# Kernel optimization log

Hardware: AMD Instinct MI355X
Metric: run time of the kernel (lower is better)

## Reference

```python
import jax, jax.numpy as jnp
import numpy as np
import math

N = 12288
D = 64
SCALE0 = math.log(10.0)


def lorentz_linear(x, W, b, scale):
    # x: [N, D] -> nn.Linear then Lorentz re-normalization onto the hyperboloid
    h = x @ W.T + b
    time = jax.nn.sigmoid(h[:, :1]) * jnp.exp(scale) + 1.1  # [N, 1]
    xn = h[:, 1:]  # spatial components [N, D-1]
    sq = jnp.clip(jnp.sum(xn * xn, axis=-1, keepdims=True), 1e-8, None)
    s = (time * time - 1.0) / sq
    return jnp.concatenate([time, xn * jnp.sqrt(s)], axis=-1)


def setup_inputs() -> dict:
    key = jax.random.key(0)
    ks = jax.random.split(key, 8)
    stdv = 1.0 / math.sqrt(D)
    x = jax.random.normal(ks[0], (N, D), dtype=jnp.float32)
    # sparse-ish binary adjacency stored dense (module calls adj.to_dense())
    adj = (jax.random.uniform(ks[1], (N, N)) < 0.002).astype(jnp.float32)
    W = jax.random.uniform(ks[2], (D, D), minval=-stdv, maxval=stdv, dtype=jnp.float32)
    Wq = jax.random.uniform(ks[3], (D, D), minval=-stdv, maxval=stdv, dtype=jnp.float32)
    Wk = jax.random.uniform(ks[4], (D, D), minval=-stdv, maxval=stdv, dtype=jnp.float32)
    z = jnp.zeros((D,), dtype=jnp.float32)
    sc = jnp.asarray(SCALE0, dtype=jnp.float32)
    return {
        'x': x, 'adj': adj,
        'W': W, 'b': z, 'scale': sc,
        'Wq': Wq, 'bq': z, 'scale_q': sc,
        'Wk': Wk, 'bk': z, 'scale_k': sc,
        'att_bias': jnp.asarray(20.0, dtype=jnp.float32),
        'att_scale': jnp.asarray(math.sqrt(D), dtype=jnp.float32),
    }


def reference(x, adj, W, b, scale, Wq, bq, scale_q, Wk, bk, scale_k, att_bias, att_scale):
    # LorentzLinear
    h = lorentz_linear(x, W, b, scale)  # [N, D]
    # LorentzAgg with attention
    q = lorentz_linear(h, Wq, bq, scale_q)
    k = lorentz_linear(h, Wk, bk, scale_k)
    # cinner: Lorentzian inner product matrix (negate time component of q)
    qm = jnp.concatenate([-q[:, :1], q[:, 1:]], axis=-1)
    att = 2.0 + 2.0 * (qm @ k.T)                 # [N, N]
    att = jax.nn.sigmoid(att / att_scale + att_bias)
    att = adj * att                               # mask by adjacency
    support = att @ h                             # [N, D]
    # Lorentz self-inner: inner(v,v) = -v0^2 + sum(v_rest^2); denorm = sqrt(|-inner|)
    inner = -support[:, :1] ** 2 + jnp.sum(support[:, 1:] ** 2, axis=-1, keepdims=True)
    denorm = jnp.sqrt(jnp.clip(jnp.abs(-inner), 1e-8, None))
    return support / denorm
```

## Files before the change

kernel.cpp:

```cpp
#include <hip/hip_runtime.h>
#include <math.h>

#define N   12288
#define D   64
#define CAP 96

typedef unsigned int uint4n __attribute__((ext_vector_type(4)));

__device__ __forceinline__ float wave_sum(float v) {
    #pragma unroll
    for (int m = 32; m >= 1; m >>= 1) v += __shfl_xor(v, m, 64);
    return v;
}
__device__ __forceinline__ float sigmoidf(float a) { return 1.0f / (1.0f + __expf(-a)); }

__global__ __launch_bounds__(256) void phase1_kernel(
        const float* __restrict__ x,
        const uint4n* __restrict__ adj4,
        const float* __restrict__ W,  const float* __restrict__ b,  const float* __restrict__ scale,
        const float* __restrict__ Wq, const float* __restrict__ bq, const float* __restrict__ scale_q,
        const float* __restrict__ Wk, const float* __restrict__ bk, const float* __restrict__ scale_k,
        float* __restrict__ h, float* __restrict__ qm, float* __restrict__ kmat,
        int* __restrict__ cnt, int* __restrict__ cols) {
    __shared__ float Wl [D * (D + 1)];
    __shared__ float Wql[D * (D + 1)];
    __shared__ float Wkl[D * (D + 1)];
    __shared__ unsigned short scols[4][CAP];
    __shared__ int scnt[4];

    const int tid  = threadIdx.x;
    const int lane = tid & 63;
    const int w    = tid >> 6;
    const int row  = blockIdx.x * 4 + w;

    for (int idx = tid; idx < D * D; idx += 256) {
        int d = idx >> 6, kk = idx & 63;
        Wl [d * (D + 1) + kk] = W [idx];
        Wql[d * (D + 1) + kk] = Wq[idx];
        Wkl[d * (D + 1) + kk] = Wk[idx];
    }
    if (lane == 0) scnt[w] = 0;
    __syncthreads();

    float hvv;
    {
        float xv  = x[row * D + lane];
        float acc = b[lane];
        const float* wr = &Wl[lane * (D + 1)];
        #pragma unroll
        for (int kk = 0; kk < D; ++kk)
            acc = fmaf(__shfl(xv, kk, 64), wr[kk], acc);
        float h0   = __shfl(acc, 0, 64);
        float time = __expf(scale[0]) * sigmoidf(h0) + 1.1f;
        float sq   = fmaxf(wave_sum((lane == 0) ? 0.0f : acc * acc), 1e-8f);
        float r    = sqrtf((time * time - 1.0f) / sq);
        hvv = (lane == 0) ? time : acc * r;
        h[row * D + lane] = hvv;
    }

    {
        float accq = bq[lane], acck = bk[lane];
        const float* wq = &Wql[lane * (D + 1)];
        const float* wk = &Wkl[lane * (D + 1)];
        #pragma unroll
        for (int kk = 0; kk < D; ++kk) {
            float xk = __shfl(hvv, kk, 64);
            accq = fmaf(xk, wq[kk], accq);
            acck = fmaf(xk, wk[kk], acck);
        }
        {
            float h0   = __shfl(accq, 0, 64);
            float time = __expf(scale_q[0]) * sigmoidf(h0) + 1.1f;
            float sq   = fmaxf(wave_sum((lane == 0) ? 0.0f : accq * accq), 1e-8f);
            float r    = sqrtf((time * time - 1.0f) / sq);
            qm[row * D + lane] = (lane == 0) ? -time : accq * r;
        }
        {
            float h0   = __shfl(acck, 0, 64);
            float time = __expf(scale_k[0]) * sigmoidf(h0) + 1.1f;
            float sq   = fmaxf(wave_sum((lane == 0) ? 0.0f : acck * acck), 1e-8f);
            float r    = sqrtf((time * time - 1.0f) / sq);
            kmat[row * D + lane] = (lane == 0) ? time : acck * r;
        }
    }

    {
        const uint4n* rp = adj4 + (size_t)row * (N / 4);
        #pragma unroll 4
        for (int it = 0; it < (N / 4) / 64; ++it) {
            int t = it * 64 + lane;
            uint4n v = __builtin_nontemporal_load(&rp[t]);
            if ((v.x | v.y | v.z | v.w) != 0u) {
                unsigned e[4] = {v.x, v.y, v.z, v.w};
                #pragma unroll
                for (int c = 0; c < 4; ++c) {
                    if (e[c] != 0u) {
                        int pos = atomicAdd(&scnt[w], 1);
                        if (pos < CAP) scols[w][pos] = (unsigned short)(t * 4 + c);
                    }
                }
            }
        }
        int m = scnt[w]; if (m > CAP) m = CAP;
        if (lane == 0) cnt[row] = m;
        for (int n = lane; n < m; n += 64)
            cols[row * CAP + n] = scols[w][n];
    }
}

__global__ __launch_bounds__(256) void gather_kernel(
        const float* __restrict__ qm,
        const float* __restrict__ kmat,
        const float* __restrict__ h,
        const int* __restrict__ cnt,
        const int* __restrict__ cols,
        const float* __restrict__ att_bias_p,
        const float* __restrict__ att_scale_p,
        float* __restrict__ out) {
    int lane = threadIdx.x & 63;
    int row  = blockIdx.x * 4 + (threadIdx.x >> 6);

    float qv = qm[row * D + lane];
    int m = cnt[row];
    float bias      = att_bias_p[0];
    float inv_scale = 1.0f / att_scale_p[0];

    float acc = 0.0f;
    for (int n = 0; n < m; ++n) {
        int j = cols[row * CAP + n];
        float dot = wave_sum(qv * kmat[j * D + lane]);
        float att = sigmoidf(fmaf(2.0f + 2.0f * dot, inv_scale, bias));
        acc = fmaf(att, h[j * D + lane], acc);
    }

    float contrib = (lane == 0) ? -acc * acc : acc * acc;
    float inner   = wave_sum(contrib);
    float denorm  = sqrtf(fmaxf(fabsf(inner), 1e-8f));
    out[row * D + lane] = acc / denorm;
}

extern "C" void kernel_launch(void* const* d_in, const int* in_sizes, int n_in,
                              void* d_out, int out_size, void* d_ws, size_t ws_size,
                              hipStream_t stream) {
    const float*  x         = (const float*)d_in[0];
    const uint4n* adj       = (const uint4n*)d_in[1];
    const float*  W         = (const float*)d_in[2];
    const float*  b         = (const float*)d_in[3];
    const float*  scale     = (const float*)d_in[4];
    const float*  Wq        = (const float*)d_in[5];
    const float*  bq        = (const float*)d_in[6];
    const float*  scale_q   = (const float*)d_in[7];
    const float*  Wk        = (const float*)d_in[8];
    const float*  bk        = (const float*)d_in[9];
    const float*  scale_k   = (const float*)d_in[10];
    const float*  att_bias  = (const float*)d_in[11];
    const float*  att_scale = (const float*)d_in[12];
    float* out = (float*)d_out;

    float* h    = (float*)d_ws;
    float* qm   = h    + (size_t)N * D;
    float* kmat = qm   + (size_t)N * D;
    int*   cnt  = (int*)(kmat + (size_t)N * D);
    int*   cols = cnt + N;

    phase1_kernel<<<N / 4, 256, 0, stream>>>(x, adj, W, b, scale,
                                             Wq, bq, scale_q, Wk, bk, scale_k,
                                             h, qm, kmat, cnt, cols);
    gather_kernel<<<N / 4, 256, 0, stream>>>(qm, kmat, h, cnt, cols,
                                             att_bias, att_scale, out);
}
```

Measured before the change: 851.5 us.

## Fuse adjacency scan into gather kernel with one block per row

Moves the dense adjacency row scan out of the linear kernel and into the gather kernel. Each 256-thread block now scans one row and keeps the neighbor list in shared memory. The four waves then split the neighbor loop and reduce their partial sums through shared memory. This drops the global cols/cnt round trip and spreads the scan of the 600MB adjacency over more waves per row. The cost is an extra block barrier, a cross-wave reduction, and three idle waves during the final normalization.

```diff
diff --git a/kernel.cpp b/kernel.cpp
--- a/kernel.cpp
+++ b/kernel.cpp
@@ -14,19 +14,15 @@
 }
 __device__ __forceinline__ float sigmoidf(float a) { return 1.0f / (1.0f + __expf(-a)); }
 
-__global__ __launch_bounds__(256) void phase1_kernel(
+__global__ __launch_bounds__(256) void linear_kernel(
         const float* __restrict__ x,
-        const uint4n* __restrict__ adj4,
         const float* __restrict__ W,  const float* __restrict__ b,  const float* __restrict__ scale,
         const float* __restrict__ Wq, const float* __restrict__ bq, const float* __restrict__ scale_q,
         const float* __restrict__ Wk, const float* __restrict__ bk, const float* __restrict__ scale_k,
-        float* __restrict__ h, float* __restrict__ qm, float* __restrict__ kmat,
-        int* __restrict__ cnt, int* __restrict__ cols) {
+        float* __restrict__ h, float* __restrict__ qm, float* __restrict__ kmat) {
     __shared__ float Wl [D * (D + 1)];
     __shared__ float Wql[D * (D + 1)];
     __shared__ float Wkl[D * (D + 1)];
-    __shared__ unsigned short scols[4][CAP];
-    __shared__ int scnt[4];
 
     const int tid  = threadIdx.x;
     const int lane = tid & 63;
@@ -39,7 +35,6 @@
         Wql[d * (D + 1) + kk] = Wq[idx];
         Wkl[d * (D + 1) + kk] = Wk[idx];
     }
-    if (lane == 0) scnt[w] = 0;
     __syncthreads();
 
     float hvv;
@@ -83,60 +78,68 @@
             kmat[row * D + lane] = (lane == 0) ? time : acck * r;
         }
     }
+}
 
-    {
-        const uint4n* rp = adj4 + (size_t)row * (N / 4);
-        #pragma unroll 4
-        for (int it = 0; it < (N / 4) / 64; ++it) {
-            int t = it * 64 + lane;
-            uint4n v = __builtin_nontemporal_load(&rp[t]);
-            if ((v.x | v.y | v.z | v.w) != 0u) {
-                unsigned e[4] = {v.x, v.y, v.z, v.w};
-                #pragma unroll
-                for (int c = 0; c < 4; ++c) {
-                    if (e[c] != 0u) {
-                        int pos = atomicAdd(&scnt[w], 1);
-                        if (pos < CAP) scols[w][pos] = (unsigned short)(t * 4 + c);
-                    }
+__global__ __launch_bounds__(256) void adj_gather_kernel(
+        const uint4n* __restrict__ adj4,
+        const float* __restrict__ qm,
+        const float* __restrict__ kmat,
+        const float* __restrict__ h,
+        const float* __restrict__ att_bias_p,
+        const float* __restrict__ att_scale_p,
+        float* __restrict__ out) {
+    __shared__ int scols[CAP];
+    __shared__ int scnt;
+    __shared__ float sacc[4][D];
+
+    int tid  = threadIdx.x;
+    int row  = blockIdx.x;
+    if (tid == 0) scnt = 0;
+    __syncthreads();
+
+    const uint4n* rowp = adj4 + (size_t)row * (N / 4);
+    #pragma unroll
+    for (int it = 0; it < (N / 4) / 256; ++it) {
+        int t = it * 256 + tid;
+        uint4n v = __builtin_nontemporal_load(&rowp[t]);
+        if ((v.x | v.y | v.z | v.w) != 0u) {
+            unsigned e[4] = {v.x, v.y, v.z, v.w};
+            #pragma unroll
+            for (int c = 0; c < 4; ++c) {
+                if (e[c] != 0u) {
+                    int pos = atomicAdd(&scnt, 1);
+                    if (pos < CAP) scols[pos] = t * 4 + c;
                 }
             }
         }
-        int m = scnt[w]; if (m > CAP) m = CAP;
-        if (lane == 0) cnt[row] = m;
-        for (int n = lane; n < m; n += 64)
-            cols[row * CAP + n] = scols[w][n];
     }
-}
+    __syncthreads();
 
-__global__ __launch_bounds__(256) void gather_kernel(
-        const float* __restrict__ qm,
-        const float* __restrict__ kmat,
-        const float* __restrict__ h,
-        const int* __restrict__ cnt,
-        const int* __restrict__ cols,
-        const float* __restrict__ att_bias_p,
-        const float* __restrict__ att_scale_p,
-        float* __restrict__ out) {
-    int lane = threadIdx.x & 63;
-    int row  = blockIdx.x * 4 + (threadIdx.x >> 6);
+    int m = scnt; if (m > CAP) m = CAP;
+    int lane = tid & 63;
+    int w    = tid >> 6;
 
-    float qv = qm[row * D + lane];
-    int m = cnt[row];
+    float qv        = qm[row * D + lane];
     float bias      = att_bias_p[0];
     float inv_scale = 1.0f / att_scale_p[0];
 
     float acc = 0.0f;
-    for (int n = 0; n < m; ++n) {
-        int j = cols[row * CAP + n];
+    for (int n = w; n < m; n += 4) {
+        int j = scols[n];
         float dot = wave_sum(qv * kmat[j * D + lane]);
         float att = sigmoidf(fmaf(2.0f + 2.0f * dot, inv_scale, bias));
         acc = fmaf(att, h[j * D + lane], acc);
     }
+    sacc[w][lane] = acc;
+    __syncthreads();
 
-    float contrib = (lane == 0) ? -acc * acc : acc * acc;
-    float inner   = wave_sum(contrib);
-    float denorm  = sqrtf(fmaxf(fabsf(inner), 1e-8f));
-    out[row * D + lane] = acc / denorm;
+    if (w == 0) {
+        float total = sacc[0][lane] + sacc[1][lane] + sacc[2][lane] + sacc[3][lane];
+        float contrib = (lane == 0) ? -total * total : total * total;
+        float inner   = wave_sum(contrib);
+        float denorm  = sqrtf(fmaxf(fabsf(inner), 1e-8f));
+        out[row * D + lane] = total / denorm;
+    }
 }
 
 extern "C" void kernel_launch(void* const* d_in, const int* in_sizes, int n_in,
@@ -158,14 +161,12 @@
     float* out = (float*)d_out;
 
     float* h    = (float*)d_ws;
-    float* qm   = h    + (size_t)N * D;
-    float* kmat = qm   + (size_t)N * D;
-    int*   cnt  = (int*)(kmat + (size_t)N * D);
-    int*   cols = cnt + N;
+    float* qm   = h  + (size_t)N * D;
+    float* kmat = qm + (size_t)N * D;
 
-    phase1_kernel<<<N / 4, 256, 0, stream>>>(x, adj, W, b, scale,
+    linear_kernel<<<N / 4, 256, 0, stream>>>(x, W, b, scale,
                                              Wq, bq, scale_q, Wk, bk, scale_k,
-                                             h, qm, kmat, cnt, cols);
-    gather_kernel<<<N / 4, 256, 0, stream>>>(qm, kmat, h, cnt, cols,
+                                             h, qm, kmat);
+    adj_gather_kernel<<<N, 256, 0, stream>>>(adj, qm, kmat, h,
                                              att_bias, att_scale, out);
 }
```

Result: faster. 800.0 us (-6.0%).

## Split adjacency scan into grid-stride streaming kernel with batched loads

Applied to the files above, without the earlier changes.

Moves the dense adjacency scan out of the per-row linear kernel into its own kernel. That kernel uses 1024 blocks in a flat grid-stride sweep and keeps 8 nontemporal 16-byte loads in flight per thread. Nonzeros are appended through global atomics on per-row counters, which the linear kernel now zeroes. The aim is higher memory-level parallelism on the 600MB adjacency read. In exchange it adds a kernel launch, global atomics, and a column order within each row that is no longer deterministic.

```diff
diff --git a/kernel.cpp b/kernel.cpp
--- a/kernel.cpp
+++ b/kernel.cpp
@@ -1,9 +1,15 @@
 #include <hip/hip_runtime.h>
 #include <math.h>
 
-#define N   12288
-#define D   64
-#define CAP 96
+#define N    12288
+#define D    64
+#define CAP  96
+
+#define TOTAL4 (N * (N / 4))
+#define SG     1024
+#define STH    (SG * 256)
+#define SB     8
+#define SIT    (TOTAL4 / (STH * SB))
 
 typedef unsigned int uint4n __attribute__((ext_vector_type(4)));
 
@@ -14,24 +20,23 @@
 }
 __device__ __forceinline__ float sigmoidf(float a) { return 1.0f / (1.0f + __expf(-a)); }
 
-__global__ __launch_bounds__(256) void phase1_kernel(
+__global__ __launch_bounds__(256) void linear_kernel(
         const float* __restrict__ x,
-        const uint4n* __restrict__ adj4,
         const float* __restrict__ W,  const float* __restrict__ b,  const float* __restrict__ scale,
         const float* __restrict__ Wq, const float* __restrict__ bq, const float* __restrict__ scale_q,
         const float* __restrict__ Wk, const float* __restrict__ bk, const float* __restrict__ scale_k,
         float* __restrict__ h, float* __restrict__ qm, float* __restrict__ kmat,
-        int* __restrict__ cnt, int* __restrict__ cols) {
+        int* __restrict__ cnt) {
     __shared__ float Wl [D * (D + 1)];
     __shared__ float Wql[D * (D + 1)];
     __shared__ float Wkl[D * (D + 1)];
-    __shared__ unsigned short scols[4][CAP];
-    __shared__ int scnt[4];
 
     const int tid  = threadIdx.x;
     const int lane = tid & 63;
     const int w    = tid >> 6;
     const int row  = blockIdx.x * 4 + w;
+
+    if (lane == 0) cnt[row] = 0;
 
     for (int idx = tid; idx < D * D; idx += 256) {
         int d = idx >> 6, kk = idx & 63;
@@ -39,7 +44,6 @@
         Wql[d * (D + 1) + kk] = Wq[idx];
         Wkl[d * (D + 1) + kk] = Wk[idx];
     }
-    if (lane == 0) scnt[w] = 0;
     __syncthreads();
 
     float hvv;
@@ -83,28 +87,35 @@
             kmat[row * D + lane] = (lane == 0) ? time : acck * r;
         }
     }
+}
 
-    {
-        const uint4n* rp = adj4 + (size_t)row * (N / 4);
-        #pragma unroll 4
-        for (int it = 0; it < (N / 4) / 64; ++it) {
-            int t = it * 64 + lane;
-            uint4n v = __builtin_nontemporal_load(&rp[t]);
-            if ((v.x | v.y | v.z | v.w) != 0u) {
-                unsigned e[4] = {v.x, v.y, v.z, v.w};
+__global__ __launch_bounds__(256) void scan_kernel(
+        const uint4n* __restrict__ adj4,
+        int* __restrict__ cnt,
+        int* __restrict__ cols) {
+    const int gid = blockIdx.x * 256 + threadIdx.x;
+    for (int it = 0; it < SIT; ++it) {
+        uint4n v[SB];
+        #pragma unroll
+        for (int i = 0; i < SB; ++i)
+            v[i] = __builtin_nontemporal_load(&adj4[(size_t)(it * SB + i) * STH + gid]);
+        #pragma unroll
+        for (int i = 0; i < SB; ++i) {
+            uint4n u = v[i];
+            if ((u.x | u.y | u.z | u.w) != 0u) {
+                int t   = (it * SB + i) * STH + gid;
+                int row = t / (N / 4);
+                int jb  = (t - row * (N / 4)) * 4;
+                unsigned e[4] = {u.x, u.y, u.z, u.w};
                 #pragma unroll
                 for (int c = 0; c < 4; ++c) {
                     if (e[c] != 0u) {
-                        int pos = atomicAdd(&scnt[w], 1);
-                        if (pos < CAP) scols[w][pos] = (unsigned short)(t * 4 + c);
+                        int pos = atomicAdd(&cnt[row], 1);
+                        if (pos < CAP) cols[row * CAP + pos] = jb + c;
                     }
                 }
             }
         }
-        int m = scnt[w]; if (m > CAP) m = CAP;
-        if (lane == 0) cnt[row] = m;
-        for (int n = lane; n < m; n += 64)
-            cols[row * CAP + n] = scols[w][n];
     }
 }
 
@@ -121,7 +132,7 @@
     int row  = blockIdx.x * 4 + (threadIdx.x >> 6);
 
     float qv = qm[row * D + lane];
-    int m = cnt[row];
+    int m = cnt[row]; if (m > CAP) m = CAP;
     float bias      = att_bias_p[0];
     float inv_scale = 1.0f / att_scale_p[0];
 
@@ -163,9 +174,10 @@
     int*   cnt  = (int*)(kmat + (size_t)N * D);
     int*   cols = cnt + N;
 
-    phase1_kernel<<<N / 4, 256, 0, stream>>>(x, adj, W, b, scale,
+    linear_kernel<<<N / 4, 256, 0, stream>>>(x, W, b, scale,
                                              Wq, bq, scale_q, Wk, bk, scale_k,
-                                             h, qm, kmat, cnt, cols);
+                                             h, qm, kmat, cnt);
+    scan_kernel<<<SG, 256, 0, stream>>>(adj, cnt, cols);
     gather_kernel<<<N / 4, 256, 0, stream>>>(qm, kmat, h, cnt, cols,
                                              att_bias, att_scale, out);
 }
```

Result: no change. 860.8 us (+1.1%).
